# Kernel tuning notes

Measured on AMD Instinct MI355X. Metric: run time of the kernel, lower is better.

The kernel has to match this reference:

```python
import jax, jax.numpy as jnp
import numpy as np

# module hyperparameters (from init_kwargs)
R_MIN, R_MAX = 0.01, 0.6
RH, RW = 64, 64          # retinal_H, retinal_W
H, W = 64, 128           # output pooled H, W
UFR, UFT = 4, 4          # upsampling factors


def make_grid(weight):
    """Vectorized version of get_grid. weight: [B,2].
    Faithful to source: only the top-left [H, W] corner of the
    [H*UFR, W*UFT] grid is written; the rest (torch.empty in the
    original) is set to 0 here for determinism."""
    i = jnp.arange(H, dtype=jnp.float32)
    j = jnp.arange(W, dtype=jnp.float32)
    xg = (i - (H // 2)) / (H / 2.0)
    yg = (j - (W // 2)) / (W / 2.0)
    xx, yy = jnp.meshgrid(xg, yg, indexing="ij")  # [H,W]
    # clamp radius to avoid log(0) = -inf at the center pixel; the resulting
    # coordinate is far out of [-1,1] and gets border-clamped either way.
    logr = jnp.log(jnp.maximum(jnp.sqrt(xx ** 2 + yy ** 2), 1e-12))  # [H,W]
    lo = jnp.log(weight[:, 0] * R_MIN)[:, None, None]  # [B,1,1]
    hi = jnp.log(weight[:, 1] * R_MAX)[:, None, None]  # [B,1,1]
    r = RH * (logr[None] - lo) / (hi - lo)             # [B,H,W]
    a = jnp.arctan2(yy, xx)
    a = jnp.where(a > 0, a, 2.0 * np.pi + a)
    t = 0.5 * a * RW / np.pi                           # [H,W]
    gx = jnp.broadcast_to((t / (RW / 2.0) - 1.0)[None], r.shape)
    gy = r / (RH / 2.0) - 1.0
    small = jnp.stack([gx, gy], axis=-1)               # [B,H,W,2]
    grid = jnp.zeros((weight.shape[0], H * UFR, W * UFT, 2), jnp.float32)
    return grid.at[:, :H, :W, :].set(small)


def grid_sample_border(x, grid):
    """torch.F.grid_sample, mode=bilinear, padding_mode=border, align_corners=False.
    x: [B,C,Hin,Win], grid: [B,Hg,Wg,2] -> [B,C,Hg,Wg]."""
    B, C, Hin, Win = x.shape
    gx, gy = grid[..., 0], grid[..., 1]
    ix = jnp.clip(((gx + 1.0) * Win - 1.0) * 0.5, 0.0, Win - 1.0)
    iy = jnp.clip(((gy + 1.0) * Hin - 1.0) * 0.5, 0.0, Hin - 1.0)
    x0f = jnp.floor(ix)
    y0f = jnp.floor(iy)
    wx = (ix - x0f)[..., None]
    wy = (iy - y0f)[..., None]
    x0 = jnp.clip(x0f.astype(jnp.int32), 0, Win - 1)
    y0 = jnp.clip(y0f.astype(jnp.int32), 0, Hin - 1)
    x1 = jnp.clip(x0 + 1, 0, Win - 1)
    y1 = jnp.clip(y0 + 1, 0, Hin - 1)
    bidx = jnp.arange(B)[:, None, None]
    gather = lambda yi, xi: x[bidx, :, yi, xi]  # [B,Hg,Wg,C]
    out = (gather(y0, x0) * (1 - wx) * (1 - wy)
           + gather(y0, x1) * wx * (1 - wy)
           + gather(y1, x0) * (1 - wx) * wy
           + gather(y1, x1) * wx * wy)
    return jnp.transpose(out, (0, 3, 1, 2))  # [B,C,Hg,Wg]


def setup_inputs() -> dict:
    key = jax.random.key(0)
    k1, k2, k3, k4, k5, k6 = jax.random.split(key, 6)
    B, C, Hin, Win = 8, 64, 224, 224
    Cmid = C // 2  # int(channel * r)
    return {
        "x": jax.random.normal(k1, (B, C, Hin, Win), jnp.float32),
        "l_t_prev": jax.random.uniform(k2, (B, 2), jnp.float32),
        "w1": jax.random.normal(k3, (C, Cmid), jnp.float32) * 0.1,
        "b1": jnp.zeros((Cmid,), jnp.float32),
        "w2": jax.random.normal(k4, (Cmid, 2), jnp.float32) * 0.1,
        "b2": jnp.zeros((2,), jnp.float32),
    }


def reference(x, l_t_prev, w1, b1, w2, b2):
    # att: global avg pool -> fc -> sigmoid
    branch = x.mean(axis=(2, 3))                              # [B,C]
    weight = jax.nn.sigmoid(jax.nn.relu(branch @ w1 + b1) @ w2 + b2)  # [B,2]
    grid = make_grid(weight) + l_t_prev[:, None, None, :]     # [B,Hg,Wg,2]
    sampled = grid_sample_border(x, grid)                     # [B,C,Hg,Wg]
    B, C = sampled.shape[:2]
    pooled = sampled.reshape(B, C, H, UFR, W, UFT).mean(axis=(3, 5))  # AvgPool2d([UFR,UFT])
    return pooled, weight
```

## Files before the change

### kernel.cpp

```cpp
#include <hip/hip_runtime.h>
#include <math.h>

#define B 8
#define C 64
#define HIN 224
#define WIN 224
#define PLANE (HIN*WIN)
#define PLANE4 (PLANE/4)
#define QUART (PLANE4/4)
#define OH 64
#define OW 128
#define OUT_PER_BC (OH*OW)
#define NGRID (OH*OW)
#define POOLED_SIZE (B*C*OH*OW)

#define WS_PARTIAL 0
#define WS_WEIGHT 2048
#define WS_COORDS 4096

#define PI_F 3.14159265358979323846f

__global__ __launch_bounds__(256) void k1_gap(const float* __restrict__ x,
                                              float* __restrict__ ws) {
    int blk = blockIdx.x;
    int bc  = blk >> 2, q = blk & 3;
    const float4* p = (const float4*)x + (size_t)bc * PLANE4 + q * QUART;
    int tid = threadIdx.x;
    float s = 0.f;
#pragma unroll
    for (int k = 0; k < 12; ++k) {
        float4 v = p[tid + k * 256];
        s += (v.x + v.y) + (v.z + v.w);
    }
    if (tid < QUART - 12 * 256) {
        float4 v = p[tid + 12 * 256];
        s += (v.x + v.y) + (v.z + v.w);
    }
    for (int off = 32; off; off >>= 1) s += __shfl_down(s, off, 64);
    __shared__ float lds[4];
    if ((tid & 63) == 0) lds[tid >> 6] = s;
    __syncthreads();
    if (tid == 0) ws[WS_PARTIAL + blk] = lds[0] + lds[1] + lds[2] + lds[3];
}

__global__ __launch_bounds__(256) void k2_mlp(const float* __restrict__ w1,
                                              const float* __restrict__ b1,
                                              const float* __restrict__ w2,
                                              const float* __restrict__ b2,
                                              float* __restrict__ ws,
                                              float* __restrict__ out_weight) {
    __shared__ float branch[B * C];
    __shared__ float hidden[B * 32];
    int tid = threadIdx.x;
    for (int i = tid; i < B * C; i += 256) {
        const float* pp = ws + WS_PARTIAL + i * 4;
        branch[i] = (pp[0] + pp[1] + pp[2] + pp[3]) * (1.0f / PLANE);
    }
    __syncthreads();
    {
        int b = tid >> 5, m = tid & 31;
        float h = b1[m];
        for (int c = 0; c < C; ++c) h += branch[b * C + c] * w1[c * 32 + m];
        hidden[b * 32 + m] = h > 0.f ? h : 0.f;
    }
    __syncthreads();
    if (tid < 16) {
        int bb = tid >> 1, k = tid & 1;
        float s = b2[k];
        for (int mm = 0; mm < 32; ++mm) s += hidden[bb * 32 + mm] * w2[mm * 2 + k];
        float wv = 1.f / (1.f + expf(-s));
        ws[WS_WEIGHT + tid] = wv;
        out_weight[tid] = wv;
    }
}

__global__ __launch_bounds__(256) void k2b_coords(const float* __restrict__ wgt,
                                                  const float* __restrict__ l_t,
                                                  float2* __restrict__ coords) {
    int p = blockIdx.x * 256 + threadIdx.x;
    int b = p >> 13;
    int rem = p & 8191;
    int i = rem >> 7;
    int j = rem & 127;
    float w0 = wgt[b * 2 + 0];
    float w1v = wgt[b * 2 + 1];
    float lo = logf(w0 * 0.01f);
    float hi = logf(w1v * 0.6f);
    float xg = (float)(i - 32) * (1.f / 32.f);
    float yg = (float)(j - 64) * (1.f / 64.f);
    float rr = sqrtf(xg * xg + yg * yg);
    float logr = logf(fmaxf(rr, 1e-12f));
    float r = 64.f * (logr - lo) / (hi - lo);
    float a = atan2f(yg, xg);
    if (!(a > 0.f)) a = 2.f * PI_F + a;
    float t = 0.5f * a * 64.f / PI_F;
    float gx = t * (1.f / 32.f) - 1.f + l_t[b * 2 + 0];
    float gy = r * (1.f / 32.f) - 1.f + l_t[b * 2 + 1];
    float ix = ((gx + 1.f) * (float)WIN - 1.f) * 0.5f;
    float iy = ((gy + 1.f) * (float)HIN - 1.f) * 0.5f;
    ix = fminf(fmaxf(ix, 0.f), (float)(WIN - 1));
    iy = fminf(fmaxf(iy, 0.f), (float)(HIN - 1));
    coords[p] = make_float2(ix, iy);
}

__device__ __forceinline__ float bilinear(const float* __restrict__ p,
                                          float ix, float iy) {
    float x0f = floorf(ix), y0f = floorf(iy);
    int x0 = (int)x0f, y0 = (int)y0f;
    float wx = ix - x0f, wy = iy - y0f;
    int x1 = min(x0 + 1, WIN - 1);
    int y1 = min(y0 + 1, HIN - 1);
    const float* r0 = p + y0 * WIN;
    const float* r1 = p + y1 * WIN;
    float v00 = r0[x0], v01 = r0[x1], v10 = r1[x0], v11 = r1[x1];
    float v0 = v00 + (v01 - v00) * wx;
    float v1 = v10 + (v11 - v10) * wx;
    return v0 + (v1 - v0) * wy;
}

__global__ __launch_bounds__(256) void k3_sample(const float* __restrict__ x,
                                                 const float* __restrict__ l_t,
                                                 const float2* __restrict__ coords,
                                                 float* __restrict__ out) {
    int bc = blockIdx.x;
    int b = bc >> 6;
    int tid = threadIdx.x;
    const float* plane = x + (size_t)bc * PLANE;
    float* o = out + (size_t)bc * OUT_PER_BC;

    float gx = l_t[b * 2 + 0], gy = l_t[b * 2 + 1];
    float ixc = fminf(fmaxf(((gx + 1.f) * (float)WIN - 1.f) * 0.5f, 0.f), (float)(WIN - 1));
    float iyc = fminf(fmaxf(((gy + 1.f) * (float)HIN - 1.f) * 0.5f, 0.f), (float)(HIN - 1));
    float vconst = bilinear(plane, ixc, iyc);

#pragma unroll
    for (int k = 0; k < 32; ++k) {
        int oi = tid + k * 256;
        int h = oi >> 7, w = oi & 127;
        if (!(h < 16 && w < 32)) o[oi] = vconst;
    }

    const float2* cb = coords + b * NGRID;
#pragma unroll
    for (int rr = 0; rr < 2; ++rr) {
        int oi = tid + rr * 256;
        int h = oi >> 5, w = oi & 31;
        float acc = 0.f;
#pragma unroll
        for (int di = 0; di < 4; ++di) {
            const float2* cr = cb + (4 * h + di) * 128 + 4 * w;
#pragma unroll
            for (int dj = 0; dj < 4; ++dj) {
                float2 cxy = cr[dj];
                acc += bilinear(plane, cxy.x, cxy.y);
            }
        }
        o[h * 128 + w] = acc * (1.f / 16.f);
    }
}

extern "C" void kernel_launch(void* const* d_in, const int* in_sizes, int n_in,
                              void* d_out, int out_size, void* d_ws, size_t ws_size,
                              hipStream_t stream) {
    const float* x   = (const float*)d_in[0];
    const float* l_t = (const float*)d_in[1];
    const float* w1  = (const float*)d_in[2];
    const float* b1  = (const float*)d_in[3];
    const float* w2  = (const float*)d_in[4];
    const float* b2  = (const float*)d_in[5];
    float* out = (float*)d_out;
    float* ws  = (float*)d_ws;

    k1_gap<<<dim3(B * C * 4), dim3(256), 0, stream>>>(x, ws);
    k2_mlp<<<dim3(1), dim3(256), 0, stream>>>(w1, b1, w2, b2, ws, out + POOLED_SIZE);
    k2b_coords<<<dim3(NGRID * B / 256), dim3(256), 0, stream>>>(ws + WS_WEIGHT, l_t,
                                                                (float2*)(ws + WS_COORDS));
    k3_sample<<<dim3(B * C), dim3(256), 0, stream>>>(x, l_t,
                                                     (const float2*)(ws + WS_COORDS), out);
}
```

Measured before the change: 178.8 us.

## Fuse constant border fill into GAP kernel and MLP into coords kernel

Moves the constant-value fill of the non-corner output region into the global-average-pool kernel, so it runs alongside the read of x instead of in the sampling kernel. The tiny single-block MLP is recomputed redundantly in each of the 256 coords blocks, which removes one launch and a serial dependency. The sampling kernel becomes a flat per-output kernel over only the 16x32 corner, reading coordinates as float4. This cuts kernel launches from four to three and spreads the fill writes across more blocks, at the cost of redundant MLP work per block.

```diff
diff --git a/kernel.cpp b/kernel.cpp
--- a/kernel.cpp
+++ b/kernel.cpp
@@ -15,93 +15,9 @@
 #define POOLED_SIZE (B*C*OH*OW)
 
 #define WS_PARTIAL 0
-#define WS_WEIGHT 2048
 #define WS_COORDS 4096
 
 #define PI_F 3.14159265358979323846f
-
-__global__ __launch_bounds__(256) void k1_gap(const float* __restrict__ x,
-                                              float* __restrict__ ws) {
-    int blk = blockIdx.x;
-    int bc  = blk >> 2, q = blk & 3;
-    const float4* p = (const float4*)x + (size_t)bc * PLANE4 + q * QUART;
-    int tid = threadIdx.x;
-    float s = 0.f;
-#pragma unroll
-    for (int k = 0; k < 12; ++k) {
-        float4 v = p[tid + k * 256];
-        s += (v.x + v.y) + (v.z + v.w);
-    }
-    if (tid < QUART - 12 * 256) {
-        float4 v = p[tid + 12 * 256];
-        s += (v.x + v.y) + (v.z + v.w);
-    }
-    for (int off = 32; off; off >>= 1) s += __shfl_down(s, off, 64);
-    __shared__ float lds[4];
-    if ((tid & 63) == 0) lds[tid >> 6] = s;
-    __syncthreads();
-    if (tid == 0) ws[WS_PARTIAL + blk] = lds[0] + lds[1] + lds[2] + lds[3];
-}
-
-__global__ __launch_bounds__(256) void k2_mlp(const float* __restrict__ w1,
-                                              const float* __restrict__ b1,
-                                              const float* __restrict__ w2,
-                                              const float* __restrict__ b2,
-                                              float* __restrict__ ws,
-                                              float* __restrict__ out_weight) {
-    __shared__ float branch[B * C];
-    __shared__ float hidden[B * 32];
-    int tid = threadIdx.x;
-    for (int i = tid; i < B * C; i += 256) {
-        const float* pp = ws + WS_PARTIAL + i * 4;
-        branch[i] = (pp[0] + pp[1] + pp[2] + pp[3]) * (1.0f / PLANE);
-    }
-    __syncthreads();
-    {
-        int b = tid >> 5, m = tid & 31;
-        float h = b1[m];
-        for (int c = 0; c < C; ++c) h += branch[b * C + c] * w1[c * 32 + m];
-        hidden[b * 32 + m] = h > 0.f ? h : 0.f;
-    }
-    __syncthreads();
-    if (tid < 16) {
-        int bb = tid >> 1, k = tid & 1;
-        float s = b2[k];
-        for (int mm = 0; mm < 32; ++mm) s += hidden[bb * 32 + mm] * w2[mm * 2 + k];
-        float wv = 1.f / (1.f + expf(-s));
-        ws[WS_WEIGHT + tid] = wv;
-        out_weight[tid] = wv;
-    }
-}
-
-__global__ __launch_bounds__(256) void k2b_coords(const float* __restrict__ wgt,
-                                                  const float* __restrict__ l_t,
-                                                  float2* __restrict__ coords) {
-    int p = blockIdx.x * 256 + threadIdx.x;
-    int b = p >> 13;
-    int rem = p & 8191;
-    int i = rem >> 7;
-    int j = rem & 127;
-    float w0 = wgt[b * 2 + 0];
-    float w1v = wgt[b * 2 + 1];
-    float lo = logf(w0 * 0.01f);
-    float hi = logf(w1v * 0.6f);
-    float xg = (float)(i - 32) * (1.f / 32.f);
-    float yg = (float)(j - 64) * (1.f / 64.f);
-    float rr = sqrtf(xg * xg + yg * yg);
-    float logr = logf(fmaxf(rr, 1e-12f));
-    float r = 64.f * (logr - lo) / (hi - lo);
-    float a = atan2f(yg, xg);
-    if (!(a > 0.f)) a = 2.f * PI_F + a;
-    float t = 0.5f * a * 64.f / PI_F;
-    float gx = t * (1.f / 32.f) - 1.f + l_t[b * 2 + 0];
-    float gy = r * (1.f / 32.f) - 1.f + l_t[b * 2 + 1];
-    float ix = ((gx + 1.f) * (float)WIN - 1.f) * 0.5f;
-    float iy = ((gy + 1.f) * (float)HIN - 1.f) * 0.5f;
-    ix = fminf(fmaxf(ix, 0.f), (float)(WIN - 1));
-    iy = fminf(fmaxf(iy, 0.f), (float)(HIN - 1));
-    coords[p] = make_float2(ix, iy);
-}
 
 __device__ __forceinline__ float bilinear(const float* __restrict__ p,
                                           float ix, float iy) {
@@ -118,45 +34,136 @@
     return v0 + (v1 - v0) * wy;
 }
 
-__global__ __launch_bounds__(256) void k3_sample(const float* __restrict__ x,
+__global__ __launch_bounds__(256) void k1_gap_fill(const float* __restrict__ x,
+                                                   const float* __restrict__ l_t,
+                                                   float* __restrict__ ws,
+                                                   float* __restrict__ out) {
+    int blk = blockIdx.x;
+    int bc  = blk >> 2, q = blk & 3;
+    const float* plane = x + (size_t)bc * PLANE;
+    const float4* p = (const float4*)plane + q * QUART;
+    int tid = threadIdx.x;
+    float s = 0.f;
+#pragma unroll
+    for (int k = 0; k < 12; ++k) {
+        float4 v = p[tid + k * 256];
+        s += (v.x + v.y) + (v.z + v.w);
+    }
+    if (tid < QUART - 12 * 256) {
+        float4 v = p[tid + 12 * 256];
+        s += (v.x + v.y) + (v.z + v.w);
+    }
+
+    {
+        int b = bc >> 6;
+        float gx = l_t[2 * b], gy = l_t[2 * b + 1];
+        float ixc = fminf(fmaxf(((gx + 1.f) * (float)WIN - 1.f) * 0.5f, 0.f), (float)(WIN - 1));
+        float iyc = fminf(fmaxf(((gy + 1.f) * (float)HIN - 1.f) * 0.5f, 0.f), (float)(HIN - 1));
+        float vc = bilinear(plane, ixc, iyc);
+        float4 v4 = make_float4(vc, vc, vc, vc);
+        float4* o4 = (float4*)(out + (size_t)bc * OUT_PER_BC);
+        int end = q * 480 + 480;
+        for (int it = q * 480 + tid; it < end; it += 256) {
+            int off;
+            if (it < 384) {
+                int r = it / 24;
+                off = r * 32 + 8 + (it - r * 24);
+            } else {
+                int t2 = it - 384;
+                off = (16 + (t2 >> 5)) * 32 + (t2 & 31);
+            }
+            o4[off] = v4;
+        }
+    }
+
+    for (int off = 32; off; off >>= 1) s += __shfl_down(s, off, 64);
+    __shared__ float lds[4];
+    if ((tid & 63) == 0) lds[tid >> 6] = s;
+    __syncthreads();
+    if (tid == 0) ws[WS_PARTIAL + blk] = lds[0] + lds[1] + lds[2] + lds[3];
+}
+
+__global__ __launch_bounds__(256) void k2_coords(const float* __restrict__ w1,
+                                                 const float* __restrict__ b1,
+                                                 const float* __restrict__ w2,
+                                                 const float* __restrict__ b2,
                                                  const float* __restrict__ l_t,
+                                                 float* __restrict__ ws,
+                                                 float* __restrict__ out_weight) {
+    __shared__ float branch[B * C];
+    __shared__ float hidden[256];
+    __shared__ float wv[16];
+    int tid = threadIdx.x;
+    for (int i = tid; i < B * C; i += 256) {
+        const float* pp = ws + WS_PARTIAL + i * 4;
+        branch[i] = (pp[0] + pp[1] + pp[2] + pp[3]) * (1.0f / PLANE);
+    }
+    __syncthreads();
+    {
+        int bb = tid >> 5, m = tid & 31;
+        float h = b1[m];
+#pragma unroll 8
+        for (int c = 0; c < C; ++c) h += branch[bb * C + c] * w1[c * 32 + m];
+        hidden[tid] = fmaxf(h, 0.f);
+    }
+    __syncthreads();
+    if (tid < 16) {
+        int bb = tid >> 1, k = tid & 1;
+        float s = b2[k];
+#pragma unroll
+        for (int m = 0; m < 32; ++m) s += hidden[bb * 32 + m] * w2[m * 2 + k];
+        float v = 1.f / (1.f + expf(-s));
+        wv[tid] = v;
+        if (blockIdx.x == 0) out_weight[tid] = v;
+    }
+    __syncthreads();
+
+    int p = blockIdx.x * 256 + tid;
+    int b = p >> 13;
+    int rem = p & 8191;
+    int i = rem >> 7;
+    int j = rem & 127;
+    float lo = logf(wv[b * 2 + 0] * 0.01f);
+    float hi = logf(wv[b * 2 + 1] * 0.6f);
+    float xg = (float)(i - 32) * (1.f / 32.f);
+    float yg = (float)(j - 64) * (1.f / 64.f);
+    float rr = sqrtf(xg * xg + yg * yg);
+    float logr = logf(fmaxf(rr, 1e-12f));
+    float r = 64.f * (logr - lo) / (hi - lo);
+    float a = atan2f(yg, xg);
+    if (!(a > 0.f)) a = 2.f * PI_F + a;
+    float t = 0.5f * a * 64.f / PI_F;
+    float gx = t * (1.f / 32.f) - 1.f + l_t[b * 2 + 0];
+    float gy = r * (1.f / 32.f) - 1.f + l_t[b * 2 + 1];
+    float ix = ((gx + 1.f) * (float)WIN - 1.f) * 0.5f;
+    float iy = ((gy + 1.f) * (float)HIN - 1.f) * 0.5f;
+    ix = fminf(fmaxf(ix, 0.f), (float)(WIN - 1));
+    iy = fminf(fmaxf(iy, 0.f), (float)(HIN - 1));
+    ((float2*)(ws + WS_COORDS))[p] = make_float2(ix, iy);
+}
+
+__global__ __launch_bounds__(256) void k3_corner(const float* __restrict__ x,
                                                  const float2* __restrict__ coords,
                                                  float* __restrict__ out) {
-    int bc = blockIdx.x;
-    int b = bc >> 6;
-    int tid = threadIdx.x;
-    const float* plane = x + (size_t)bc * PLANE;
-    float* o = out + (size_t)bc * OUT_PER_BC;
-
-    float gx = l_t[b * 2 + 0], gy = l_t[b * 2 + 1];
-    float ixc = fminf(fmaxf(((gx + 1.f) * (float)WIN - 1.f) * 0.5f, 0.f), (float)(WIN - 1));
-    float iyc = fminf(fmaxf(((gy + 1.f) * (float)HIN - 1.f) * 0.5f, 0.f), (float)(HIN - 1));
-    float vconst = bilinear(plane, ixc, iyc);
-
+    int o = blockIdx.x * 256 + threadIdx.x;
+    int b = o >> 15;
+    int c = (o >> 9) & 63;
+    int h = (o >> 5) & 15;
+    int w = o & 31;
+    const float* plane = x + (size_t)((b << 6) | c) * PLANE;
+    const float2* cb = coords + ((size_t)b << 13);
+    float acc = 0.f;
 #pragma unroll
-    for (int k = 0; k < 32; ++k) {
-        int oi = tid + k * 256;
-        int h = oi >> 7, w = oi & 127;
-        if (!(h < 16 && w < 32)) o[oi] = vconst;
+    for (int di = 0; di < 4; ++di) {
+        const float4* cr = (const float4*)(cb + ((4 * h + di) << 7) + (w << 2));
+        float4 q0 = cr[0];
+        float4 q1 = cr[1];
+        acc += bilinear(plane, q0.x, q0.y);
+        acc += bilinear(plane, q0.z, q0.w);
+        acc += bilinear(plane, q1.x, q1.y);
+        acc += bilinear(plane, q1.z, q1.w);
     }
-
-    const float2* cb = coords + b * NGRID;
-#pragma unroll
-    for (int rr = 0; rr < 2; ++rr) {
-        int oi = tid + rr * 256;
-        int h = oi >> 5, w = oi & 31;
-        float acc = 0.f;
-#pragma unroll
-        for (int di = 0; di < 4; ++di) {
-            const float2* cr = cb + (4 * h + di) * 128 + 4 * w;
-#pragma unroll
-            for (int dj = 0; dj < 4; ++dj) {
-                float2 cxy = cr[dj];
-                acc += bilinear(plane, cxy.x, cxy.y);
-            }
-        }
-        o[h * 128 + w] = acc * (1.f / 16.f);
-    }
+    out[((size_t)((b << 6) | c) << 13) + (h << 7) + w] = acc * (1.f / 16.f);
 }
 
 extern "C" void kernel_launch(void* const* d_in, const int* in_sizes, int n_in,
@@ -171,10 +178,8 @@
     float* out = (float*)d_out;
     float* ws  = (float*)d_ws;
 
-    k1_gap<<<dim3(B * C * 4), dim3(256), 0, stream>>>(x, ws);
-    k2_mlp<<<dim3(1), dim3(256), 0, stream>>>(w1, b1, w2, b2, ws, out + POOLED_SIZE);
-    k2b_coords<<<dim3(NGRID * B / 256), dim3(256), 0, stream>>>(ws + WS_WEIGHT, l_t,
-                                                                (float2*)(ws + WS_COORDS));
-    k3_sample<<<dim3(B * C), dim3(256), 0, stream>>>(x, l_t,
-                                                     (const float2*)(ws + WS_COORDS), out);
+    k1_gap_fill<<<dim3(B * C * 4), dim3(256), 0, stream>>>(x, l_t, ws, out);
+    k2_coords<<<dim3(256), dim3(256), 0, stream>>>(w1, b1, w2, b2, l_t, ws,
+                                                   out + POOLED_SIZE);
+    k3_corner<<<dim3(1024), dim3(256), 0, stream>>>(x, (const float2*)(ws + WS_COORDS), out);
 }
```

Result: no change. 180.3 us (+0.8%).
